# Kernel tuning notes

Measured on AMD Instinct MI355X. Metric: run time of the kernel, lower is better.

## Reference

```python
import jax, jax.numpy as jnp
import numpy as np

D_MODEL = 2048
D_COMPARE = 2048
D_MEMORY = 2048
N_HEADS = 16
KV_HEADS = 4
KV_REPEAT = N_HEADS // KV_HEADS          # 4
C_HD = D_COMPARE // N_HEADS              # 128 compare head dim
M_HD = D_MEMORY // N_HEADS               # 128 memory head dim
TOTAL_OUT = D_COMPARE + KV_HEADS * C_HD + KV_HEADS * M_HD  # 3072


def setup_inputs() -> dict:
    key = jax.random.key(0)
    ks = jax.random.split(key, 5)
    b, t = 2, 2048
    x = jax.random.normal(ks[0], (b, t, D_MODEL), dtype=jnp.float32)
    s_in = 1.0 / np.sqrt(D_MODEL)
    s_out = 1.0 / np.sqrt(D_MEMORY)
    in_w = jax.random.uniform(ks[1], (TOTAL_OUT, D_MODEL), jnp.float32, -s_in, s_in)
    in_b = jax.random.uniform(ks[2], (TOTAL_OUT,), jnp.float32, -s_in, s_in)
    out_w = jax.random.uniform(ks[3], (D_MODEL, D_MEMORY), jnp.float32, -s_out, s_out)
    out_b = jax.random.uniform(ks[4], (D_MODEL,), jnp.float32, -s_out, s_out)
    return {"x": x, "in_w": in_w, "in_b": in_b, "out_w": out_w, "out_b": out_b}


def reference(x, in_w, in_b, out_w, out_b):
    b, t, _ = x.shape
    packed = jnp.einsum("btd,od->bto", x, in_w) + in_b          # [b,t,TOTAL_OUT]
    q, k, v = jnp.split(packed, [D_COMPARE, D_COMPARE + KV_HEADS * C_HD], axis=-1)
    # q: [b, kv, rep, t, hd] -- head h maps to kv group h // KV_REPEAT
    # (torch repeat_interleave on KV head dim == grouped reshape of q heads)
    q = q.reshape(b, t, KV_HEADS, KV_REPEAT, C_HD).transpose(0, 2, 3, 1, 4)
    k = k.reshape(b, t, KV_HEADS, C_HD).transpose(0, 2, 1, 3)   # [b,kv,t,hd]
    v = v.reshape(b, t, KV_HEADS, M_HD).transpose(0, 2, 1, 3)   # [b,kv,t,mhd]
    scale = 1.0 / np.sqrt(C_HD)
    scores = jnp.einsum("bgrqd,bgkd->bgrqk", q, k) * scale      # [b,kv,rep,t,t]
    attn = jax.nn.softmax(scores, axis=-1)
    y = jnp.einsum("bgrqk,bgkd->bgrqd", attn, v)                # [b,kv,rep,t,mhd]
    y = y.transpose(0, 3, 1, 2, 4).reshape(b, t, D_MEMORY)      # heads back in order
    return jnp.einsum("btm,dm->btd", y, out_w) + out_b
```

## Files before the change

kernel.cpp:

```cpp
#include <hip/hip_runtime.h>
#include <hip/hip_bf16.h>
#include <stdint.h>

#define DEV __device__ __forceinline__

typedef __attribute__((ext_vector_type(8))) short bf16x8;
typedef __attribute__((ext_vector_type(4))) float f32x4;

DEV unsigned short f2bf(float f) {
  unsigned u = __builtin_bit_cast(unsigned, f);
  unsigned r = u + 0x7FFF + ((u >> 16) & 1);
  return (unsigned short)(r >> 16);
}

DEV unsigned short f2bfh(float f) {
  __bf16 h = (__bf16)f;
  return __builtin_bit_cast(unsigned short, h);
}

typedef __attribute__((address_space(1))) void gvoid;
typedef __attribute__((address_space(3))) void lvoid;

DEV void g2l16(const void* g, void* l) {
  __builtin_amdgcn_global_load_lds((gvoid*)g, (lvoid*)l, 16, 0, 0);
}

#define MFMA16(a, b, c) __builtin_amdgcn_mfma_f32_16x16x32_bf16(a, b, c, 0, 0, 0)

__global__ void k_cvt3(const float* __restrict__ x, unsigned short* __restrict__ xo, int nx4,
                       const float* __restrict__ w, unsigned short* __restrict__ wo, int nw4,
                       const float* __restrict__ v, unsigned short* __restrict__ vo, int nv4) {
  int i = blockIdx.x * blockDim.x + threadIdx.x;
  int stride = gridDim.x * blockDim.x;
  int tot = nx4 + nw4 + nv4;
  for (; i < tot; i += stride) {
    const float* src; unsigned short* dst; int j = i;
    if (j < nx4) { src = x; dst = xo; }
    else if ((j -= nx4) < nw4) { src = w; dst = wo; }
    else { j -= nw4; src = v; dst = vo; }
    float4 val = reinterpret_cast<const float4*>(src)[j];
    ushort4 o;
    o.x = f2bf(val.x); o.y = f2bf(val.y); o.z = f2bf(val.z); o.w = f2bf(val.w);
    reinterpret_cast<ushort4*>(dst)[j] = o;
  }
}

template<bool BF16OUT>
__global__ __launch_bounds__(256, 2) void k_gemm(
    const unsigned short* __restrict__ A, const unsigned short* __restrict__ B,
    const float* __restrict__ bias, void* __restrict__ C,
    int M, int N, int K) {
  __shared__ unsigned short As[128 * 32];
  __shared__ unsigned short Bs[128 * 32];
  int tid = threadIdx.x;
  int lane = tid & 63, wid = tid >> 6;
  int bm = blockIdx.y * 128, bn = blockIdx.x * 128;
  int wm = (wid >> 1) * 64, wn = (wid & 1) * 64;
  int row16 = lane & 15, kq = lane >> 4;
  f32x4 acc[4][4] = {};
  int r = tid >> 2, c = (tid & 3) * 8;
  const unsigned short* Ag = A + (size_t)(bm + r) * K + c;
  const unsigned short* Bg = B + (size_t)(bn + r) * K + c;
  for (int k0 = 0; k0 < K; k0 += 32) {
    g2l16(Ag + k0, &As[tid * 8]);
    g2l16(Ag + (size_t)64 * K + k0, &As[2048 + tid * 8]);
    g2l16(Bg + k0, &Bs[tid * 8]);
    g2l16(Bg + (size_t)64 * K + k0, &Bs[2048 + tid * 8]);
    __syncthreads();
    bf16x8 a[4], b[4];
#pragma unroll
    for (int m = 0; m < 4; m++) a[m] = *(const bf16x8*)&As[(wm + m * 16 + row16) * 32 + kq * 8];
#pragma unroll
    for (int n = 0; n < 4; n++) b[n] = *(const bf16x8*)&Bs[(wn + n * 16 + row16) * 32 + kq * 8];
    __builtin_amdgcn_s_setprio(1);
#pragma unroll
    for (int m = 0; m < 4; m++)
#pragma unroll
      for (int n = 0; n < 4; n++)
        acc[m][n] = MFMA16(a[m], b[n], acc[m][n]);
    __builtin_amdgcn_s_setprio(0);
    __syncthreads();
  }
#pragma unroll
  for (int n = 0; n < 4; n++) {
    int col = bn + wn + n * 16 + row16;
    float bv = bias[col];
#pragma unroll
    for (int m = 0; m < 4; m++) {
      int rw = bm + wm + m * 16 + kq * 4;
#pragma unroll
      for (int j = 0; j < 4; j++) {
        float v = acc[m][n][j] + bv;
        if (BF16OUT) ((unsigned short*)C)[(size_t)(rw + j) * N + col] = f2bf(v);
        else         ((float*)C)[(size_t)(rw + j) * N + col] = v;
      }
    }
  }
}

__global__ void k_vt(const unsigned short* __restrict__ packed, unsigned short* __restrict__ vT) {
  __shared__ unsigned short tile[64][136];
  int g = blockIdx.y;
  int b = g >> 2, kv = g & 3;
  int t0 = blockIdx.x * 64;
  int tid = threadIdx.x;
#pragma unroll
  for (int i = 0; i < 4; i++) {
    int tl = i * 16 + (tid >> 4);
    int d0 = (tid & 15) * 8;
    bf16x8 v = *(const bf16x8*)&packed[(size_t)(b * 2048 + t0 + tl) * 3072 + 2560 + kv * 128 + d0];
    *(bf16x8*)&tile[tl][d0] = v;
  }
  __syncthreads();
  int d = tid >> 1, ts = (tid & 1) * 32;
  size_t obase = (size_t)(g * 128 + d) * 2048 + t0 + ts;
#pragma unroll
  for (int j = 0; j < 4; j++) {
    bf16x8 o;
#pragma unroll
    for (int e = 0; e < 8; e++) o[e] = (short)tile[ts + j * 8 + e][d];
    *(bf16x8*)&vT[obase + j * 8] = o;
  }
}

__global__ __launch_bounds__(512, 4) void k_flash(
    const unsigned short* __restrict__ packed,
    const unsigned short* __restrict__ vT,
    unsigned short* __restrict__ Y) {
  __shared__ unsigned short Ks[2][64 * 128];
  __shared__ unsigned short Vs[128 * 64];
  __shared__ unsigned short Ps[8][16 * 72];
  __shared__ float Axc[8][16];
  int tid = threadIdx.x, lane = tid & 63, wid = tid >> 6;
  int row16 = lane & 15, kq = lane >> 4;
  int r3 = row16 & 7;
  int g = blockIdx.x;
  int s8 = g & 7;
  int b = s8 >> 2, kv = s8 & 3;
  int w = g >> 3;
  int h = kv * 4 + (w & 3);
  int qt = w >> 2;
  size_t prow = (size_t)b * 2048;

  unsigned short* Q = &Ks[0][0];
  {
    int rr = tid >> 4;
    int cc = ((tid & 15) ^ (rr & 7)) * 8;
    const unsigned short* qg = packed + (prow + qt * 128 + rr) * 3072 + h * 128 + cc;
#pragma unroll
    for (int i = 0; i < 4; i++)
      g2l16(qg + (size_t)i * 32 * 3072, &Q[i * 4096 + tid * 8]);
  }
  asm volatile("s_waitcnt vmcnt(0)" ::: "memory");
  __builtin_amdgcn_s_barrier();
  bf16x8 q[4];
#pragma unroll
  for (int kc = 0; kc < 4; kc++)
    q[kc] = *(const bf16x8*)&Q[(wid * 16 + row16) * 128 + (((kc * 4 + kq) ^ r3) * 8)];
  asm volatile("s_waitcnt lgkmcnt(0)" ::: "memory");
  __builtin_amdgcn_sched_barrier(0);
  __builtin_amdgcn_s_barrier();

  const unsigned short* kg0 = packed + prow * 3072 + 2048 + kv * 128;
  const unsigned short* vg0 = vT + (size_t)(b * 4 + kv) * 128 * 2048;
  int krr = tid >> 4;
  int kcc = ((tid & 15) ^ (krr & 7)) * 8;
  int vrr = tid >> 3;
  int vcc = ((tid & 7) ^ (vrr & 7)) * 8;

  auto stageK = [&](int t, int kbuf) {
    const unsigned short* kg = kg0 + (size_t)(t * 64 + krr) * 3072 + kcc;
#pragma unroll
    for (int i = 0; i < 2; i++)
      g2l16(kg + (size_t)i * 32 * 3072, &Ks[kbuf][i * 4096 + tid * 8]);
  };
  auto stageV = [&](int t) {
    const unsigned short* vg = vg0 + (size_t)vrr * 2048 + t * 64 + vcc;
#pragma unroll
    for (int i = 0; i < 2; i++)
      g2l16(vg + (size_t)i * 64 * 2048, &Vs[i * 4096 + tid * 8]);
  };

  stageK(0, 0);
  stageV(0);
  asm volatile("s_waitcnt vmcnt(2)" ::: "memory");
  __builtin_amdgcn_s_barrier();

  f32x4 o[8] = {};
  f32x4 ls = {};
  float mr = -1e30f;
  const float sc2 = 0.08838834764831845f * 1.4426950408889634f;
  bf16x8 ones;
#pragma unroll
  for (int e = 0; e < 8; e++) ones[e] = (short)0x3F80;

  for (int t = 0; t < 32; t++) {
    int kb = t & 1;
    int tn = t < 31 ? t + 1 : 31;

    f32x4 st[4];
#pragma unroll
    for (int mk = 0; mk < 4; mk++) {
      st[mk] = f32x4{0.f, 0.f, 0.f, 0.f};
      bf16x8 bk[4];
#pragma unroll
      for (int kc = 0; kc < 4; kc++)
        bk[kc] = *(const bf16x8*)&Ks[kb][(mk * 16 + row16) * 128 + (((kc * 4 + kq) ^ r3) * 8)];
      __builtin_amdgcn_s_setprio(1);
#pragma unroll
      for (int kc = 0; kc < 4; kc++)
        st[mk] = MFMA16(bk[kc], q[kc], st[mk]);
      __builtin_amdgcn_s_setprio(0);
    }

    stageK(tn, kb ^ 1);

    float a0 = fmaxf(fmaxf(st[0][0], st[0][1]), fmaxf(st[0][2], st[0][3]));
    float a1 = fmaxf(fmaxf(st[1][0], st[1][1]), fmaxf(st[1][2], st[1][3]));
    float a2 = fmaxf(fmaxf(st[2][0], st[2][1]), fmaxf(st[2][2], st[2][3]));
    float a3 = fmaxf(fmaxf(st[3][0], st[3][1]), fmaxf(st[3][2], st[3][3]));
    float p = fmaxf(fmaxf(a0, a1), fmaxf(a2, a3));
    p = fmaxf(p, __shfl_xor(p, 16));
    p = fmaxf(p, __shfl_xor(p, 32));
    p *= sc2;
    if (!__all(p <= mr + 8.f)) {
      float mn = fmaxf(mr, p);
      float al = exp2f(mr - mn);
      mr = mn;
      if (lane < 16) Axc[wid][row16] = al;
      float alo[4];
#pragma unroll
      for (int j = 0; j < 4; j++) alo[j] = Axc[wid][kq * 4 + j];
#pragma unroll
      for (int np = 0; np < 8; np++)
#pragma unroll
        for (int j = 0; j < 4; j++) o[np][j] *= alo[j];
#pragma unroll
      for (int j = 0; j < 4; j++) ls[j] *= alo[j];
    }
    float nm = -mr;
#pragma unroll
    for (int mk = 0; mk < 4; mk++)
#pragma unroll
      for (int j = 0; j < 4; j++)
        st[mk][j] = exp2f(fmaf(st[mk][j], sc2, nm));

#pragma unroll
    for (int mk = 0; mk < 4; mk++) {
      ushort4 pw;
      pw.x = f2bfh(st[mk][0]); pw.y = f2bfh(st[mk][1]);
      pw.z = f2bfh(st[mk][2]); pw.w = f2bfh(st[mk][3]);
      *(ushort4*)&Ps[wid][row16 * 72 + mk * 16 + kq * 4] = pw;
    }
    bf16x8 pf[2];
#pragma unroll
    for (int k2 = 0; k2 < 2; k2++)
      pf[k2] = *(const bf16x8*)&Ps[wid][row16 * 72 + k2 * 32 + kq * 8];

    asm volatile("s_waitcnt vmcnt(2)" ::: "memory");
    __builtin_amdgcn_s_barrier();

#pragma unroll
    for (int np = 0; np < 8; np++) {
      int vrow = np * 16 + row16;
      bf16x8 bv0 = *(const bf16x8*)&Vs[vrow * 64 + ((kq ^ r3) * 8)];
      bf16x8 bv1 = *(const bf16x8*)&Vs[vrow * 64 + (((4 + kq) ^ r3) * 8)];
      __builtin_amdgcn_s_setprio(1);
      o[np] = MFMA16(pf[0], bv0, o[np]);
      o[np] = MFMA16(pf[1], bv1, o[np]);
      __builtin_amdgcn_s_setprio(0);
    }
    ls = MFMA16(pf[0], ones, ls);
    ls = MFMA16(pf[1], ones, ls);

    __builtin_amdgcn_s_barrier();
    stageV(tn);
    asm volatile("s_waitcnt vmcnt(2)" ::: "memory");
    __builtin_amdgcn_s_barrier();
  }
  asm volatile("s_waitcnt vmcnt(0)" ::: "memory");

#pragma unroll
  for (int j = 0; j < 4; j++) {
    float inv = 1.f / ls[j];
    size_t orow = prow + (size_t)qt * 128 + wid * 16 + kq * 4 + j;
#pragma unroll
    for (int np = 0; np < 8; np++)
      Y[orow * 2048 + h * 128 + np * 16 + row16] = f2bfh(o[np][j] * inv);
  }
}

extern "C" void kernel_launch(void* const* d_in, const int* in_sizes, int n_in,
                              void* d_out, int out_size, void* d_ws, size_t ws_size,
                              hipStream_t stream) {
  const float* x     = (const float*)d_in[0];
  const float* in_w  = (const float*)d_in[1];
  const float* in_b  = (const float*)d_in[2];
  const float* out_w = (const float*)d_in[3];
  const float* out_b = (const float*)d_in[4];
  float* out = (float*)d_out;

  unsigned short* xb     = (unsigned short*)d_ws;
  unsigned short* wb     = xb + 8388608;
  unsigned short* owb    = wb + 6291456;
  unsigned short* packed = owb + 4194304;
  unsigned short* vt     = packed + 12582912;
  unsigned short* y      = vt + 2097152;

  k_cvt3<<<dim3(2048), dim3(256), 0, stream>>>(x, xb, 8388608 / 4,
                                               in_w, wb, 6291456 / 4,
                                               out_w, owb, 4194304 / 4);

  k_gemm<true><<<dim3(24, 32), dim3(256), 0, stream>>>(xb, wb, in_b, packed, 4096, 3072, 2048);
  k_vt<<<dim3(32, 8), dim3(256), 0, stream>>>(packed, vt);
  k_flash<<<dim3(512), dim3(512), 0, stream>>>(packed, vt, y);
  k_gemm<false><<<dim3(16, 32), dim3(256), 0, stream>>>(y, owb, out_b, out, 4096, 2048, 2048);
}
```

Measured before the change: 226.3 us.

## Switch flash attention to 32x32x16 MFMA with 4 waves of 32 query rows

Rewrites the flash-attention kernel to use 32x32x16 bf16 MFMA tiles, with each of 4 waves owning 32 query rows instead of 8 waves owning 16. The row sum is now computed with scalar adds and a cross-lane shuffle instead of extra MFMAs against a ones vector. The LDS swizzles for Q, K, V and P are changed to match the new fragment layout. The aim is fewer MFMA and LDS instructions per FLOP and the removal of the extra row-sum MFMAs, at the cost of more registers per thread and fewer threads per block.

```diff
diff --git a/kernel.cpp b/kernel.cpp
--- a/kernel.cpp
+++ b/kernel.cpp
@@ -6,6 +6,7 @@
 
 typedef __attribute__((ext_vector_type(8))) short bf16x8;
 typedef __attribute__((ext_vector_type(4))) float f32x4;
+typedef __attribute__((ext_vector_type(16))) float f32x16;
 
 DEV unsigned short f2bf(float f) {
   unsigned u = __builtin_bit_cast(unsigned, f);
@@ -26,6 +27,7 @@
 }
 
 #define MFMA16(a, b, c) __builtin_amdgcn_mfma_f32_16x16x32_bf16(a, b, c, 0, 0, 0)
+#define MFMA32(a, b, c) __builtin_amdgcn_mfma_f32_32x32x16_bf16(a, b, c, 0, 0, 0)
 
 __global__ void k_cvt3(const float* __restrict__ x, unsigned short* __restrict__ xo, int nx4,
                        const float* __restrict__ w, unsigned short* __restrict__ wo, int nw4,
@@ -123,17 +125,18 @@
   }
 }
 
-__global__ __launch_bounds__(512, 4) void k_flash(
+__global__ __launch_bounds__(256, 2) void k_flash(
     const unsigned short* __restrict__ packed,
     const unsigned short* __restrict__ vT,
     unsigned short* __restrict__ Y) {
   __shared__ unsigned short Ks[2][64 * 128];
   __shared__ unsigned short Vs[128 * 64];
-  __shared__ unsigned short Ps[8][16 * 72];
-  __shared__ float Axc[8][16];
+  __shared__ unsigned short Ps[4][32 * 64];
+  __shared__ float Axc[4][32];
   int tid = threadIdx.x, lane = tid & 63, wid = tid >> 6;
-  int row16 = lane & 15, kq = lane >> 4;
-  int r3 = row16 & 7;
+  int l31 = lane & 31, hi = lane >> 5;
+  int kx = l31 & 15;
+  int vx = l31 & 7;
   int g = blockIdx.x;
   int s8 = g & 7;
   int b = s8 >> 2, kv = s8 & 3;
@@ -145,18 +148,19 @@
   unsigned short* Q = &Ks[0][0];
   {
     int rr = tid >> 4;
-    int cc = ((tid & 15) ^ (rr & 7)) * 8;
+    int cc = ((tid & 15) ^ rr) * 8;
     const unsigned short* qg = packed + (prow + qt * 128 + rr) * 3072 + h * 128 + cc;
 #pragma unroll
-    for (int i = 0; i < 4; i++)
-      g2l16(qg + (size_t)i * 32 * 3072, &Q[i * 4096 + tid * 8]);
+    for (int i = 0; i < 8; i++)
+      g2l16(qg + (size_t)i * 16 * 3072, &Q[i * 2048 + tid * 8]);
   }
   asm volatile("s_waitcnt vmcnt(0)" ::: "memory");
   __builtin_amdgcn_s_barrier();
-  bf16x8 q[4];
-#pragma unroll
-  for (int kc = 0; kc < 4; kc++)
-    q[kc] = *(const bf16x8*)&Q[(wid * 16 + row16) * 128 + (((kc * 4 + kq) ^ r3) * 8)];
+  bf16x8 q[8];
+  int qrow = wid * 32 + l31;
+#pragma unroll
+  for (int kc = 0; kc < 8; kc++)
+    q[kc] = *(const bf16x8*)&Q[qrow * 128 + (((2 * kc + hi) ^ kx) * 8)];
   asm volatile("s_waitcnt lgkmcnt(0)" ::: "memory");
   __builtin_amdgcn_sched_barrier(0);
   __builtin_amdgcn_s_barrier();
@@ -164,129 +168,143 @@
   const unsigned short* kg0 = packed + prow * 3072 + 2048 + kv * 128;
   const unsigned short* vg0 = vT + (size_t)(b * 4 + kv) * 128 * 2048;
   int krr = tid >> 4;
-  int kcc = ((tid & 15) ^ (krr & 7)) * 8;
+  int kcc = ((tid & 15) ^ krr) * 8;
   int vrr = tid >> 3;
   int vcc = ((tid & 7) ^ (vrr & 7)) * 8;
 
   auto stageK = [&](int t, int kbuf) {
     const unsigned short* kg = kg0 + (size_t)(t * 64 + krr) * 3072 + kcc;
 #pragma unroll
-    for (int i = 0; i < 2; i++)
-      g2l16(kg + (size_t)i * 32 * 3072, &Ks[kbuf][i * 4096 + tid * 8]);
+    for (int i = 0; i < 4; i++)
+      g2l16(kg + (size_t)i * 16 * 3072, &Ks[kbuf][i * 2048 + tid * 8]);
   };
   auto stageV = [&](int t) {
     const unsigned short* vg = vg0 + (size_t)vrr * 2048 + t * 64 + vcc;
 #pragma unroll
-    for (int i = 0; i < 2; i++)
-      g2l16(vg + (size_t)i * 64 * 2048, &Vs[i * 4096 + tid * 8]);
+    for (int i = 0; i < 4; i++)
+      g2l16(vg + (size_t)i * 32 * 2048, &Vs[i * 2048 + tid * 8]);
   };
 
   stageK(0, 0);
   stageV(0);
-  asm volatile("s_waitcnt vmcnt(2)" ::: "memory");
+  asm volatile("s_waitcnt vmcnt(4)" ::: "memory");
   __builtin_amdgcn_s_barrier();
 
-  f32x4 o[8] = {};
-  f32x4 ls = {};
-  float mr = -1e30f;
+  f32x16 o[4] = {};
+  float mr = -1e30f, lr = 0.f;
   const float sc2 = 0.08838834764831845f * 1.4426950408889634f;
-  bf16x8 ones;
-#pragma unroll
-  for (int e = 0; e < 8; e++) ones[e] = (short)0x3F80;
 
   for (int t = 0; t < 32; t++) {
     int kb = t & 1;
     int tn = t < 31 ? t + 1 : 31;
 
-    f32x4 st[4];
-#pragma unroll
-    for (int mk = 0; mk < 4; mk++) {
-      st[mk] = f32x4{0.f, 0.f, 0.f, 0.f};
-      bf16x8 bk[4];
-#pragma unroll
-      for (int kc = 0; kc < 4; kc++)
-        bk[kc] = *(const bf16x8*)&Ks[kb][(mk * 16 + row16) * 128 + (((kc * 4 + kq) ^ r3) * 8)];
+    f32x16 st[2] = {};
+#pragma unroll
+    for (int kb2 = 0; kb2 < 2; kb2++) {
+      bf16x8 ak[8];
+#pragma unroll
+      for (int kc = 0; kc < 8; kc++)
+        ak[kc] = *(const bf16x8*)&Ks[kb][(kb2 * 32 + l31) * 128 + (((2 * kc + hi) ^ kx) * 8)];
       __builtin_amdgcn_s_setprio(1);
 #pragma unroll
-      for (int kc = 0; kc < 4; kc++)
-        st[mk] = MFMA16(bk[kc], q[kc], st[mk]);
+      for (int kc = 0; kc < 8; kc++)
+        st[kb2] = MFMA32(ak[kc], q[kc], st[kb2]);
       __builtin_amdgcn_s_setprio(0);
     }
 
     stageK(tn, kb ^ 1);
 
-    float a0 = fmaxf(fmaxf(st[0][0], st[0][1]), fmaxf(st[0][2], st[0][3]));
-    float a1 = fmaxf(fmaxf(st[1][0], st[1][1]), fmaxf(st[1][2], st[1][3]));
-    float a2 = fmaxf(fmaxf(st[2][0], st[2][1]), fmaxf(st[2][2], st[2][3]));
-    float a3 = fmaxf(fmaxf(st[3][0], st[3][1]), fmaxf(st[3][2], st[3][3]));
-    float p = fmaxf(fmaxf(a0, a1), fmaxf(a2, a3));
-    p = fmaxf(p, __shfl_xor(p, 16));
+    float m0 = -1e30f, m1 = -1e30f;
+#pragma unroll
+    for (int r = 0; r < 16; r += 2) {
+      m0 = fmaxf(m0, fmaxf(st[0][r], st[0][r + 1]));
+      m1 = fmaxf(m1, fmaxf(st[1][r], st[1][r + 1]));
+    }
+    float p = fmaxf(m0, m1);
     p = fmaxf(p, __shfl_xor(p, 32));
     p *= sc2;
     if (!__all(p <= mr + 8.f)) {
       float mn = fmaxf(mr, p);
       float al = exp2f(mr - mn);
       mr = mn;
-      if (lane < 16) Axc[wid][row16] = al;
-      float alo[4];
-#pragma unroll
-      for (int j = 0; j < 4; j++) alo[j] = Axc[wid][kq * 4 + j];
-#pragma unroll
-      for (int np = 0; np < 8; np++)
-#pragma unroll
-        for (int j = 0; j < 4; j++) o[np][j] *= alo[j];
-#pragma unroll
-      for (int j = 0; j < 4; j++) ls[j] *= alo[j];
+      lr *= al;
+      Axc[wid][l31] = al;
+      float alo[16];
+#pragma unroll
+      for (int r = 0; r < 16; r++)
+        alo[r] = Axc[wid][(r & 3) + 8 * (r >> 2) + 4 * hi];
+#pragma unroll
+      for (int db = 0; db < 4; db++)
+#pragma unroll
+        for (int r = 0; r < 16; r++) o[db][r] *= alo[r];
     }
     float nm = -mr;
-#pragma unroll
-    for (int mk = 0; mk < 4; mk++)
-#pragma unroll
-      for (int j = 0; j < 4; j++)
-        st[mk][j] = exp2f(fmaf(st[mk][j], sc2, nm));
-
-#pragma unroll
-    for (int mk = 0; mk < 4; mk++) {
-      ushort4 pw;
-      pw.x = f2bfh(st[mk][0]); pw.y = f2bfh(st[mk][1]);
-      pw.z = f2bfh(st[mk][2]); pw.w = f2bfh(st[mk][3]);
-      *(ushort4*)&Ps[wid][row16 * 72 + mk * 16 + kq * 4] = pw;
-    }
-    bf16x8 pf[2];
-#pragma unroll
-    for (int k2 = 0; k2 < 2; k2++)
-      pf[k2] = *(const bf16x8*)&Ps[wid][row16 * 72 + k2 * 32 + kq * 8];
-
-    asm volatile("s_waitcnt vmcnt(2)" ::: "memory");
+    float rs = 0.f;
+#pragma unroll
+    for (int kb2 = 0; kb2 < 2; kb2++) {
+      float s[4];
+#pragma unroll
+      for (int u = 0; u < 4; u++) {
+        st[kb2][4 * u + 0] = exp2f(fmaf(st[kb2][4 * u + 0], sc2, nm));
+        st[kb2][4 * u + 1] = exp2f(fmaf(st[kb2][4 * u + 1], sc2, nm));
+        st[kb2][4 * u + 2] = exp2f(fmaf(st[kb2][4 * u + 2], sc2, nm));
+        st[kb2][4 * u + 3] = exp2f(fmaf(st[kb2][4 * u + 3], sc2, nm));
+        s[u] = (st[kb2][4 * u + 0] + st[kb2][4 * u + 1]) +
+               (st[kb2][4 * u + 2] + st[kb2][4 * u + 3]);
+      }
+      rs += (s[0] + s[1]) + (s[2] + s[3]);
+    }
+    rs += __shfl_xor(rs, 32);
+    lr += rs;
+
+#pragma unroll
+    for (int kb2 = 0; kb2 < 2; kb2++)
+#pragma unroll
+      for (int u = 0; u < 4; u++) {
+        ushort4 pw;
+        pw.x = f2bfh(st[kb2][4 * u + 0]);
+        pw.y = f2bfh(st[kb2][4 * u + 1]);
+        pw.z = f2bfh(st[kb2][4 * u + 2]);
+        pw.w = f2bfh(st[kb2][4 * u + 3]);
+        *(ushort4*)&Ps[wid][l31 * 64 + (((u + 4 * kb2) ^ vx) * 8) + hi * 4] = pw;
+      }
+    bf16x8 pf[4];
+#pragma unroll
+    for (int ks = 0; ks < 4; ks++)
+      pf[ks] = *(const bf16x8*)&Ps[wid][l31 * 64 + (((2 * ks + hi) ^ vx) * 8)];
+
+    asm volatile("s_waitcnt vmcnt(4)" ::: "memory");
     __builtin_amdgcn_s_barrier();
 
 #pragma unroll
-    for (int np = 0; np < 8; np++) {
-      int vrow = np * 16 + row16;
-      bf16x8 bv0 = *(const bf16x8*)&Vs[vrow * 64 + ((kq ^ r3) * 8)];
-      bf16x8 bv1 = *(const bf16x8*)&Vs[vrow * 64 + (((4 + kq) ^ r3) * 8)];
+    for (int db = 0; db < 4; db++) {
+      bf16x8 bv[4];
+#pragma unroll
+      for (int ks = 0; ks < 4; ks++)
+        bv[ks] = *(const bf16x8*)&Vs[(32 * db + l31) * 64 + (((2 * ks + hi) ^ vx) * 8)];
       __builtin_amdgcn_s_setprio(1);
-      o[np] = MFMA16(pf[0], bv0, o[np]);
-      o[np] = MFMA16(pf[1], bv1, o[np]);
+#pragma unroll
+      for (int ks = 0; ks < 4; ks++)
+        o[db] = MFMA32(pf[ks], bv[ks], o[db]);
       __builtin_amdgcn_s_setprio(0);
     }
-    ls = MFMA16(pf[0], ones, ls);
-    ls = MFMA16(pf[1], ones, ls);
 
     __builtin_amdgcn_s_barrier();
     stageV(tn);
-    asm volatile("s_waitcnt vmcnt(2)" ::: "memory");
+    asm volatile("s_waitcnt vmcnt(4)" ::: "memory");
     __builtin_amdgcn_s_barrier();
   }
   asm volatile("s_waitcnt vmcnt(0)" ::: "memory");
 
-#pragma unroll
-  for (int j = 0; j < 4; j++) {
-    float inv = 1.f / ls[j];
-    size_t orow = prow + (size_t)qt * 128 + wid * 16 + kq * 4 + j;
-#pragma unroll
-    for (int np = 0; np < 8; np++)
-      Y[orow * 2048 + h * 128 + np * 16 + row16] = f2bfh(o[np][j] * inv);
+  Axc[wid][l31] = lr;
+#pragma unroll
+  for (int r = 0; r < 16; r++) {
+    int ql = (r & 3) + 8 * (r >> 2) + 4 * hi;
+    float inv = 1.f / Axc[wid][ql];
+    size_t orow = prow + (size_t)qt * 128 + wid * 32 + ql;
+#pragma unroll
+    for (int db = 0; db < 4; db++)
+      Y[orow * 2048 + h * 128 + db * 32 + l31] = f2bfh(o[db][r] * inv);
   }
 }
 
@@ -313,6 +331,6 @@
 
   k_gemm<true><<<dim3(24, 32), dim3(256), 0, stream>>>(xb, wb, in_b, packed, 4096, 3072, 2048);
   k_vt<<<dim3(32, 8), dim3(256), 0, stream>>>(packed, vt);
-  k_flash<<<dim3(512), dim3(512), 0, stream>>>(packed, vt, y);
+  k_flash<<<dim3(512), dim3(256), 0, stream>>>(packed, vt, y);
   k_gemm<false><<<dim3(16, 32), dim3(256), 0, stream>>>(y, owb, out_b, out, 4096, 2048, 2048);
 }
```

New measurement: 225.2 us. About the same (-0.5%).
